# Optimization experiments

Measured on AMD Instinct MI355X. Metric: run time of the kernel, lower is better.

## Reference

```python
import jax, jax.numpy as jnp
import numpy as np

EMBD = 256
HEAD = 4
HD = EMBD // HEAD  # 64
EPS = 1e-5


def setup_inputs() -> dict:
    key = jax.random.key(0)
    ks = jax.random.split(key, 12)
    s = lambda fan_in: 1.0 / np.sqrt(fan_in)
    return {
        "x": jax.random.normal(ks[0], (16, 1024, EMBD), dtype=jnp.float32),
        # attention params (stored as [in, out])
        "qkv_w": jax.random.uniform(ks[1], (EMBD, 3 * EMBD), jnp.float32, -s(EMBD), s(EMBD)),
        "qkv_b": jax.random.uniform(ks[2], (3 * EMBD,), jnp.float32, -s(EMBD), s(EMBD)),
        "out_w": jax.random.uniform(ks[3], (EMBD, EMBD), jnp.float32, -s(EMBD), s(EMBD)),
        "out_b": jax.random.uniform(ks[4], (EMBD,), jnp.float32, -s(EMBD), s(EMBD)),
        # MLP params
        "fc_w": jax.random.uniform(ks[5], (EMBD, 4 * EMBD), jnp.float32, -s(EMBD), s(EMBD)),
        "fc_b": jax.random.uniform(ks[6], (4 * EMBD,), jnp.float32, -s(EMBD), s(EMBD)),
        "proj_w": jax.random.uniform(ks[7], (4 * EMBD, EMBD), jnp.float32, -s(4 * EMBD), s(4 * EMBD)),
        "proj_b": jax.random.uniform(ks[8], (EMBD,), jnp.float32, -s(4 * EMBD), s(4 * EMBD)),
        # LayerNorm params
        "ln1_g": jnp.ones((EMBD,), jnp.float32),
        "ln1_b": jnp.zeros((EMBD,), jnp.float32),
        "ln2_g": jnp.ones((EMBD,), jnp.float32),
        "ln2_b": jnp.zeros((EMBD,), jnp.float32),
    }


def layer_norm(x, g, b):
    mu = jnp.mean(x, axis=-1, keepdims=True)
    var = jnp.mean(jnp.square(x - mu), axis=-1, keepdims=True)
    return (x - mu) * jax.lax.rsqrt(var + EPS) * g + b


def block_forward(x, qkv_w, qkv_b, out_w, out_b, fc_w, fc_b, proj_w, proj_b,
                  ln1_g, ln1_b, ln2_g, ln2_b):
    B, S, E = x.shape
    # --- attention branch ---
    h = layer_norm(x, ln1_g, ln1_b)
    qkv = h @ qkv_w + qkv_b                       # [B,S,3E]
    q, k, v = jnp.split(qkv, 3, axis=-1)
    q = q.reshape(B, S, HEAD, HD).transpose(0, 2, 1, 3)  # [B,H,S,D]
    k = k.reshape(B, S, HEAD, HD).transpose(0, 2, 1, 3)
    v = v.reshape(B, S, HEAD, HD).transpose(0, 2, 1, 3)
    att = jnp.einsum('bhqd,bhkd->bhqk', q, k) / jnp.sqrt(jnp.float32(HD))
    causal = jnp.tril(jnp.ones((S, S), dtype=bool))
    att = jnp.where(causal, att, -jnp.inf)
    att = jax.nn.softmax(att, axis=-1)
    o = jnp.einsum('bhqk,bhkd->bhqd', att, v)     # [B,H,S,D]
    o = o.transpose(0, 2, 1, 3).reshape(B, S, E)
    x = x + o @ out_w + out_b
    # --- MLP branch (dropout inactive at eval) ---
    h = layer_norm(x, ln2_g, ln2_b)
    h = jax.nn.relu(h @ fc_w + fc_b)
    x = x + h @ proj_w + proj_b
    return x


def reference(x, qkv_w, qkv_b, out_w, out_b, fc_w, fc_b, proj_w, proj_b,
              ln1_g, ln1_b, ln2_g, ln2_b):
    return block_forward(x, qkv_w, qkv_b, out_w, out_b, fc_w, fc_b,
                         proj_w, proj_b, ln1_g, ln1_b, ln2_g, ln2_b)
```

## Files before the change

### kernel.cpp

```cpp
#include <hip/hip_runtime.h>
#include <cstdint>


using f32x4 = __attribute__((ext_vector_type(4))) float;
using s16x8 = __attribute__((ext_vector_type(8))) short;
using s16x4 = __attribute__((ext_vector_type(4))) short;

__device__ inline short f2bf(float f) {
    union { float f; unsigned u; } v{f};
    unsigned r = (v.u + 0x7FFFu + ((v.u >> 16) & 1u)) >> 16;
    return (short)r;
}

__device__ inline int cvt_pk_bf16(float lo, float hi) {
    int d;
    asm("v_cvt_pk_bf16_f32 %0, %1, %2" : "=v"(d) : "v"(lo), "v"(hi));
    return d;
}
__device__ inline void swap32(int& a, int& b) {
    asm("v_permlane32_swap_b32 %0, %1" : "+v"(a), "+v"(b));
}
__device__ inline void swap16(int& a, int& b) {
    asm("v_permlane16_swap_b32 %0, %1" : "+v"(a), "+v"(b));
}

__device__ inline void gload16(const void* g, void* l) {
    __builtin_amdgcn_global_load_lds(
        (const __attribute__((address_space(1))) void*)g,
        (__attribute__((address_space(3))) void*)l, 16, 0, 0);
}

__global__ __launch_bounds__(256) void wconv_all_kernel(
    const float* __restrict__ qkv_w, const float* __restrict__ out_w,
    const float* __restrict__ fc_w,  const float* __restrict__ proj_w,
    short* __restrict__ wt_qkv, short* __restrict__ wt_out,
    short* __restrict__ wt_fc,  short* __restrict__ wt_proj)
{
    __shared__ short T[64][65];
    int id = blockIdx.x;
    const float* W; short* Wt; int K, N, nt, kt;
    if (id < 48)       { W = qkv_w;  Wt = wt_qkv;  K = 256;  N = 768;  nt = id % 12;        kt = id / 12; }
    else if (id < 64)  { W = out_w;  Wt = wt_out;  K = 256;  N = 256;  nt = (id - 48) & 3;  kt = (id - 48) >> 2; }
    else if (id < 128) { W = fc_w;   Wt = wt_fc;   K = 256;  N = 1024; nt = (id - 64) & 15; kt = (id - 64) >> 4; }
    else               { W = proj_w; Wt = wt_proj; K = 1024; N = 256;  nt = (id - 128) & 3; kt = (id - 128) >> 2; }
    int n0 = nt * 64, k0 = kt * 64;

    int tid = threadIdx.x;
    int r  = tid >> 2;
    int c  = (tid & 3) << 4;

    const float* src = W + (size_t)(k0 + r) * N + n0 + c;
#pragma unroll
    for (int u = 0; u < 4; ++u) {
        float4 v = *reinterpret_cast<const float4*>(src + u * 4);
        T[r][c + u * 4 + 0] = f2bf(v.x);
        T[r][c + u * 4 + 1] = f2bf(v.y);
        T[r][c + u * 4 + 2] = f2bf(v.z);
        T[r][c + u * 4 + 3] = f2bf(v.w);
    }
    __syncthreads();
    s16x8 o0, o1;
#pragma unroll
    for (int j = 0; j < 8; ++j) { o0[j] = T[c + j][r]; o1[j] = T[c + 8 + j][r]; }
    short* dst = Wt + (size_t)(n0 + r) * K + k0 + c;
    *reinterpret_cast<s16x8*>(dst)     = o0;
    *reinterpret_cast<s16x8*>(dst + 8) = o1;
}

__global__ __launch_bounds__(256) void ln_kernel(const float* __restrict__ x,
                                                 const float* __restrict__ gamma,
                                                 const float* __restrict__ beta,
                                                 short* __restrict__ out)
{
    int tid  = threadIdx.x;
    int lane = tid & 63;
    int row  = blockIdx.x * 4 + (tid >> 6);
    const float* xr = x + (size_t)row * 256;
    float4 v = *reinterpret_cast<const float4*>(xr + lane * 4);

    float s = v.x + v.y + v.z + v.w;
#pragma unroll
    for (int o = 32; o >= 1; o >>= 1) s += __shfl_xor(s, o);
    float mu = s * (1.0f / 256.0f);

    float dx = v.x - mu, dy = v.y - mu, dz = v.z - mu, dw = v.w - mu;
    float q = dx * dx + dy * dy + dz * dz + dw * dw;
#pragma unroll
    for (int o = 32; o >= 1; o >>= 1) q += __shfl_xor(q, o);
    float rstd = rsqrtf(q * (1.0f / 256.0f) + 1e-5f);

    float4 gv = *reinterpret_cast<const float4*>(gamma + lane * 4);
    float4 bv = *reinterpret_cast<const float4*>(beta + lane * 4);
    s16x4 ov;
    ov[0] = f2bf(dx * rstd * gv.x + bv.x);
    ov[1] = f2bf(dy * rstd * gv.y + bv.y);
    ov[2] = f2bf(dz * rstd * gv.z + bv.z);
    ov[3] = f2bf(dw * rstd * gv.w + bv.w);
    *reinterpret_cast<s16x4*>(out + (size_t)row * 256 + lane * 4) = ov;
}

template <int RELU, int RES, int OBF16, int BM, int QKV>
__global__ __launch_bounds__(256) void mgemm_kernel(const short* __restrict__ A,
                                                    const short* __restrict__ Bt,
                                                    const float* __restrict__ bias,
                                                    const float* __restrict__ R,
                                                    void* __restrict__ Cv,
                                                    short* __restrict__ vt,
                                                    int N, int K)
{
    constexpr int MI  = BM / 32;
    constexpr int ASZ = BM * 64;
    constexpr int BSZ = 128 * 64;
    __shared__ short As[2 * ASZ];
    __shared__ short Bs[2 * BSZ];

    int tid = threadIdx.x;
    int l   = tid & 63;
    int w   = tid >> 6;
    int lr  = l & 15;
    int lk8 = (l >> 4) << 3;
    int r4  = (l >> 4) << 2;
    int wr  = w >> 1, wc = w & 1;
    int bn  = blockIdx.x * 128, bm = blockIdx.y * BM;

    int scolS = ((l & 7) << 3) ^ ((l >> 3) << 3);
    int srowA = w * (BM / 4) + (l >> 3);
    int srowB = (w << 5) + (l >> 3);
    const short* pa = A  + (size_t)(bm + srowA) * K + scolS;
    const short* pb = Bt + (size_t)(bn + srowB) * K + scolS;
    short* dstA = As + w * (BM / 4) * 64;
    short* dstB = Bs + (w << 11);

    f32x4 acc[MI][4];
#pragma unroll
    for (int mi = 0; mi < MI; ++mi)
#pragma unroll
        for (int ni = 0; ni < 4; ++ni) acc[mi][ni] = (f32x4){0.f, 0.f, 0.f, 0.f};

    int swz = (lr & 7) << 3;

#pragma unroll
    for (int i = 0; i < BM / 32; ++i)
        gload16(pa + (size_t)(i * 8) * K, dstA + (i << 9));
#pragma unroll
    for (int i = 0; i < 4; ++i)
        gload16(pb + (size_t)(i * 8) * K, dstB + (i << 9));
    __syncthreads();

    int cur = 0;
    for (int k0 = 0; k0 < K; k0 += 64) {
        if (k0 + 64 < K) {
            int nxt = cur ^ 1;
#pragma unroll
            for (int i = 0; i < BM / 32; ++i)
                gload16(pa + (size_t)(i * 8) * K + k0 + 64, dstA + nxt * ASZ + (i << 9));
#pragma unroll
            for (int i = 0; i < 4; ++i)
                gload16(pb + (size_t)(i * 8) * K + k0 + 64, dstB + nxt * BSZ + (i << 9));
        }
        const short* curA = As + cur * ASZ;
        const short* curB = Bs + cur * BSZ;
#pragma unroll
        for (int ks = 0; ks < 2; ++ks) {
            s16x8 af[MI], bf[4];
#pragma unroll
            for (int mi = 0; mi < MI; ++mi) {
                int row = wr * (BM / 2) + (mi << 4) + lr;
                af[mi] = *reinterpret_cast<const s16x8*>(
                    &curA[(row << 6) + (((ks << 5) + lk8) ^ swz)]);
            }
#pragma unroll
            for (int ni = 0; ni < 4; ++ni) {
                int row = (wc << 6) + (ni << 4) + lr;
                bf[ni] = *reinterpret_cast<const s16x8*>(
                    &curB[(row << 6) + (((ks << 5) + lk8) ^ swz)]);
            }
            __builtin_amdgcn_s_setprio(1);
#pragma unroll
            for (int mi = 0; mi < MI; ++mi)
#pragma unroll
                for (int ni = 0; ni < 4; ++ni)
                    acc[mi][ni] = __builtin_amdgcn_mfma_f32_16x16x32_bf16(
                        af[mi], bf[ni], acc[mi][ni], 0, 0, 0);
            __builtin_amdgcn_s_setprio(0);
        }
        __syncthreads();
        cur ^= 1;
    }

    float bv[4];
#pragma unroll
    for (int ni = 0; ni < 4; ++ni)
        bv[ni] = bias[bn + (wc << 6) + (ni << 4) + lr];

#pragma unroll
    for (int mi = 0; mi < MI; ++mi) {
#pragma unroll
        for (int ni = 0; ni < 4; ++ni) {
            int n = bn + (wc << 6) + (ni << 4) + lr;
#pragma unroll
            for (int r = 0; r < 4; ++r) {
                int m = bm + wr * (BM / 2) + (mi << 4) + r4 + r;
                float v = acc[mi][ni][r] + bv[ni];
                if (RELU) v = fmaxf(v, 0.0f);
                if (RES)  v += R[(size_t)m * N + n];
                if (QKV) {
                    if (bn < 512) {
                        ((short*)Cv)[(size_t)m * 512 + n] = f2bf(v);
                    } else {
                        int hh = (n - 512) >> 6, dd = (n - 512) & 63;
                        int bb = m >> 10, ss = m & 1023;
                        vt[(size_t)((((bb << 2) | hh) << 6) | dd) * 1024 + ss] = f2bf(v);
                    }
                } else if (OBF16) {
                    ((short*)Cv)[(size_t)m * N + n] = f2bf(v);
                } else {
                    ((float*)Cv)[(size_t)m * N + n] = v;
                }
            }
        }
    }
}

__global__ __launch_bounds__(256) void oproj_ln_kernel(const short* __restrict__ A,
                                                       const short* __restrict__ Bt,
                                                       const float* __restrict__ bias,
                                                       const float* __restrict__ R,
                                                       float* __restrict__ x1,
                                                       short* __restrict__ h2,
                                                       const float* __restrict__ g,
                                                       const float* __restrict__ bb)
{
    constexpr int ASZ = 64 * 64;
    constexpr int BSZ = 256 * 64;
    __shared__ short As[2 * ASZ];
    __shared__ short Bs[2 * BSZ];

    int tid = threadIdx.x;
    int l   = tid & 63;
    int w   = tid >> 6;
    int lr  = l & 15;
    int lk8 = (l >> 4) << 3;
    int r4  = (l >> 4) << 2;
    int bm  = blockIdx.x * 64;

    int scolS = ((l & 7) << 3) ^ ((l >> 3) << 3);
    const short* pa = A  + (size_t)(bm + (w << 4) + (l >> 3)) * 256 + scolS;
    const short* pb = Bt + (size_t)((w << 6) + (l >> 3)) * 256 + scolS;
    short* dstA = As + (w << 10);
    short* dstB = Bs + (w << 12);

    f32x4 acc[16];
#pragma unroll
    for (int ni = 0; ni < 16; ++ni) acc[ni] = (f32x4){0.f, 0.f, 0.f, 0.f};

    int swz = (lr & 7) << 3;

#pragma unroll
    for (int i = 0; i < 2; ++i)
        gload16(pa + (size_t)(i * 8) * 256, dstA + (i << 9));
#pragma unroll
    for (int i = 0; i < 8; ++i)
        gload16(pb + (size_t)(i * 8) * 256, dstB + (i << 9));
    __syncthreads();

    int cur = 0;
    for (int k0 = 0; k0 < 256; k0 += 64) {
        if (k0 + 64 < 256) {
            int nxt = cur ^ 1;
#pragma unroll
            for (int i = 0; i < 2; ++i)
                gload16(pa + (size_t)(i * 8) * 256 + k0 + 64, dstA + nxt * ASZ + (i << 9));
#pragma unroll
            for (int i = 0; i < 8; ++i)
                gload16(pb + (size_t)(i * 8) * 256 + k0 + 64, dstB + nxt * BSZ + (i << 9));
        }
        const short* curA = As + cur * ASZ;
        const short* curB = Bs + cur * BSZ;
#pragma unroll
        for (int ks = 0; ks < 2; ++ks) {
            int arow = (w << 4) + lr;
            s16x8 af = *reinterpret_cast<const s16x8*>(
                &curA[(arow << 6) + (((ks << 5) + lk8) ^ swz)]);
            __builtin_amdgcn_s_setprio(1);
#pragma unroll
            for (int ni = 0; ni < 16; ++ni) {
                int row = (ni << 4) + lr;
                s16x8 bf = *reinterpret_cast<const s16x8*>(
                    &curB[(row << 6) + (((ks << 5) + lk8) ^ swz)]);
                acc[ni] = __builtin_amdgcn_mfma_f32_16x16x32_bf16(af, bf, acc[ni], 0, 0, 0);
            }
            __builtin_amdgcn_s_setprio(0);
        }
        __syncthreads();
        cur ^= 1;
    }

#pragma unroll
    for (int ni = 0; ni < 16; ++ni) {
        int n = (ni << 4) + lr;
        float bvx = bias[n];
#pragma unroll
        for (int r = 0; r < 4; ++r) {
            int m = bm + (w << 4) + r4 + r;
            acc[ni][r] += bvx + R[(size_t)m * 256 + n];
        }
    }
#pragma unroll
    for (int r = 0; r < 4; ++r) {
        float s = 0.0f;
#pragma unroll
        for (int ni = 0; ni < 16; ++ni) s += acc[ni][r];
        s += __shfl_xor(s, 1); s += __shfl_xor(s, 2);
        s += __shfl_xor(s, 4); s += __shfl_xor(s, 8);
        float mu = s * (1.0f / 256.0f);
        float q = 0.0f;
#pragma unroll
        for (int ni = 0; ni < 16; ++ni) {
            float d = acc[ni][r] - mu;
            q += d * d;
        }
        q += __shfl_xor(q, 1); q += __shfl_xor(q, 2);
        q += __shfl_xor(q, 4); q += __shfl_xor(q, 8);
        float rstd = rsqrtf(q * (1.0f / 256.0f) + 1e-5f);

        int m = bm + (w << 4) + r4 + r;
#pragma unroll
        for (int ni = 0; ni < 16; ++ni) {
            int n = (ni << 4) + lr;
            float v = acc[ni][r];
            x1[(size_t)m * 256 + n] = v;
            h2[(size_t)m * 256 + n] = f2bf((v - mu) * rstd * g[n] + bb[n]);
        }
    }
}

__global__ __launch_bounds__(256, 4) void attn_kernel(const short* __restrict__ qk,
                                                      const short* __restrict__ vt,
                                                      short* __restrict__ o)
{
    __shared__ short Ks[2][64 * 64];
    __shared__ short Vs[2][64 * 64];

    int bid  = blockIdx.x;
    int xcd  = bid & 7;
    int rest = bid >> 3;
    int tq   = rest & 15;
    int flip = (rest >> 5) & 1;
    int qt   = flip ? 15 - tq : tq;
    int bhg  = rest >> 4;
    int bh   = (bhg << 3) | xcd;
    int b = bh >> 2, h = bh & 3;

    int tid = threadIdx.x;
    int l   = tid & 63;
    int w   = tid >> 6;
    int lr  = l & 15;
    int g   = l >> 4;
    int lk8 = g << 3;
    int w16 = w << 4;

    int srow = (w << 3) + (l >> 3);
    int scol = ((l & 7) << 3) ^ (((l >> 3) & 7) << 3);
    const short* kgp = qk + (size_t)(b * 1024 + srow) * 512 + 256 + h * 64 + scol;
    const short* vgp = vt + (size_t)((bh << 6) + srow) * 1024 + scol;
    short* dstK = &Ks[0][(w << 3) * 64];
    short* dstV = &Vs[0][(w << 3) * 64];
    const int BUFS = 64 * 64;

    const float SC = 0.125f * 1.44269504088896f;
    int rsw = (lr & 7) << 3;

    const short* qrow = qk + (size_t)(b * 1024 + qt * 64 + w16 + lr) * 512 + h * 64;
    s16x8 qf[2];
    qf[0] = *reinterpret_cast<const s16x8*>(qrow + lk8);
    qf[1] = *reinterpret_cast<const s16x8*>(qrow + 32 + lk8);

#pragma unroll
    for (int i = 0; i < 2; ++i) {
        gload16(kgp + (size_t)(i * 32) * 512, dstK + (i << 11));
        gload16(vgp + (size_t)(i * 32) * 1024, dstV + (i << 11));
    }
    __syncthreads();

    float m = -1e30f, lsum = 0.0f;
    f32x4 oacc[4];
#pragma unroll
    for (int dt = 0; dt < 4; ++dt) oacc[dt] = (f32x4){0.f, 0.f, 0.f, 0.f};
    int qglob = qt * 64 + w16 + lr;
    int cur = 0;

    for (int kt = 0; kt <= qt; ++kt) {
        if (kt < qt) {
            int nxt = cur ^ 1;
#pragma unroll
            for (int i = 0; i < 2; ++i) {
                gload16(kgp + (size_t)((kt + 1) * 64 + i * 32) * 512,
                        dstK + nxt * BUFS + (i << 11));
                gload16(vgp + (size_t)(i * 32) * 1024 + (kt + 1) * 64,
                        dstV + nxt * BUFS + (i << 11));
            }
        }

        f32x4 s[4];
#pragma unroll
        for (int jt = 0; jt < 4; ++jt) s[jt] = (f32x4){0.f, 0.f, 0.f, 0.f};
        __builtin_amdgcn_s_setprio(1);
#pragma unroll
        for (int ks = 0; ks < 2; ++ks) {
#pragma unroll
            for (int jt = 0; jt < 4; ++jt) {
                int row = jt * 16 + lr;
                s16x8 kf = *reinterpret_cast<const s16x8*>(
                    &Ks[cur][(row << 6) + ((32 * ks + lk8) ^ rsw)]);
                s[jt] = __builtin_amdgcn_mfma_f32_16x16x32_bf16(kf, qf[ks], s[jt], 0, 0, 0);
            }
        }
        __builtin_amdgcn_s_setprio(0);
#pragma unroll
        for (int jt = 0; jt < 4; ++jt)
#pragma unroll
            for (int r = 0; r < 4; ++r) s[jt][r] *= SC;

        if (kt == qt) {
#pragma unroll
            for (int jt = 0; jt < 4; ++jt) {
                int kb = kt * 64 + jt * 16 + (g << 2);
#pragma unroll
                for (int r = 0; r < 4; ++r)
                    if (kb + r > qglob) s[jt][r] = -1e30f;
            }
        }

        float rm = fmaxf(fmaxf(s[0][0], s[0][1]), fmaxf(s[0][2], s[0][3]));
#pragma unroll
        for (int jt = 1; jt < 4; ++jt)
            rm = fmaxf(rm, fmaxf(fmaxf(s[jt][0], s[jt][1]), fmaxf(s[jt][2], s[jt][3])));
        rm = fmaxf(rm, __shfl_xor(rm, 16));
        rm = fmaxf(rm, __shfl_xor(rm, 32));
        bool big = __any(rm > m + 8.0f);
        float fct = 1.0f;
        if (big) {
            float mn = fmaxf(m, rm);
            fct = exp2f(m - mn);
            m = mn;
        }
        float ps = 0.0f;
#pragma unroll
        for (int jt = 0; jt < 4; ++jt)
#pragma unroll
            for (int r = 0; r < 4; ++r) {
                float p = exp2f(s[jt][r] - m);
                s[jt][r] = p;
                ps += p;
            }
        ps += __shfl_xor(ps, 16);
        ps += __shfl_xor(ps, 32);
        lsum = lsum * fct + ps;

        int cpk[4][2];
#pragma unroll
        for (int jt = 0; jt < 4; ++jt) {
            cpk[jt][0] = cvt_pk_bf16(s[jt][0], s[jt][1]);
            cpk[jt][1] = cvt_pk_bf16(s[jt][2], s[jt][3]);
        }

        if (big) {
#pragma unroll
            for (int r = 0; r < 4; ++r) {
                float f4 = __shfl(fct, 4 * g + r);
#pragma unroll
                for (int dt = 0; dt < 4; ++dt) oacc[dt][r] *= f4;
            }
        }

#pragma unroll
        for (int ks = 0; ks < 2; ++ks) {
            int a0 = cpk[2 * ks][0],     a1 = cpk[2 * ks][1];
            int b0 = cpk[2 * ks + 1][0], b1 = cpk[2 * ks + 1][1];
            swap32(a0, b0); swap32(a1, b1);
            swap16(a0, b0); swap16(a1, b1);
            union { int i[4]; s16x8 v; } fr;
            fr.i[0] = a0; fr.i[1] = a1; fr.i[2] = b0; fr.i[3] = b1;
            __builtin_amdgcn_s_setprio(1);
#pragma unroll
            for (int dt = 0; dt < 4; ++dt) {
                int row = dt * 16 + lr;
                s16x8 vf = *reinterpret_cast<const s16x8*>(
                    &Vs[cur][(row << 6) + ((32 * ks + lk8) ^ rsw)]);
                oacc[dt] = __builtin_amdgcn_mfma_f32_16x16x32_bf16(fr.v, vf, oacc[dt], 0, 0, 0);
            }
            __builtin_amdgcn_s_setprio(0);
        }

        if (kt < qt) {
            __syncthreads();
            cur ^= 1;
        }
    }

#pragma unroll
    for (int r = 0; r < 4; ++r) {
        float lv  = __shfl(lsum, 4 * g + r);
        float inv = 1.0f / lv;
        short* orow = o + (size_t)(b * 1024 + qt * 64 + w16 + 4 * g + r) * 256 + h * 64;
#pragma unroll
        for (int dt = 0; dt < 4; ++dt)
            orow[dt * 16 + lr] = f2bf(oacc[dt][r] * inv);
    }
}

extern "C" void kernel_launch(void* const* d_in, const int* in_sizes, int n_in,
                              void* d_out, int out_size, void* d_ws, size_t ws_size,
                              hipStream_t stream)
{
    const float* x      = (const float*)d_in[0];
    const float* qkv_w  = (const float*)d_in[1];
    const float* qkv_b  = (const float*)d_in[2];
    const float* out_w  = (const float*)d_in[3];
    const float* out_b  = (const float*)d_in[4];
    const float* fc_w   = (const float*)d_in[5];
    const float* fc_b   = (const float*)d_in[6];
    const float* proj_w = (const float*)d_in[7];
    const float* proj_b = (const float*)d_in[8];
    const float* ln1_g  = (const float*)d_in[9];
    const float* ln1_b  = (const float*)d_in[10];
    const float* ln2_g  = (const float*)d_in[11];
    const float* ln2_b  = (const float*)d_in[12];
    float* out = (float*)d_out;

    short* ws = (short*)d_ws;
    short* wt_qkv  = ws;
    short* wt_out  = ws + 196608;
    short* wt_fc   = ws + 262144;
    short* wt_proj = ws + 524288;
    short* bufA    = ws + 786432;
    short* qk_buf  = ws + 4980736;
    short* vt_buf  = ws + 13369344;
    short* h3_buf  = ws + 4980736;

    dim3 blk(256);

    wconv_all_kernel<<<dim3(192), blk, 0, stream>>>(
        qkv_w, out_w, fc_w, proj_w, wt_qkv, wt_out, wt_fc, wt_proj);
    ln_kernel<<<dim3(4096), blk, 0, stream>>>(x, ln1_g, ln1_b, bufA);
    mgemm_kernel<0, 0, 1, 128, 1><<<dim3(6, 128), blk, 0, stream>>>(
        bufA, wt_qkv, qkv_b, nullptr, qk_buf, vt_buf, 768, 256);
    attn_kernel<<<dim3(1024), blk, 0, stream>>>(qk_buf, vt_buf, bufA);
    oproj_ln_kernel<<<dim3(256), blk, 0, stream>>>(
        bufA, wt_out, out_b, x, out, bufA, ln2_g, ln2_b);
    mgemm_kernel<1, 0, 1, 128, 0><<<dim3(8, 128), blk, 0, stream>>>(
        bufA, wt_fc, fc_b, nullptr, h3_buf, nullptr, 1024, 256);
    mgemm_kernel<0, 1, 0, 64, 0><<<dim3(2, 256), blk, 0, stream>>>(
        h3_buf, wt_proj, proj_b, out, out, nullptr, 256, 1024);
}
```

Baseline: 132.3 us.

## Merge weight prep with LN1, single-buffer K=256 GEMMs, retile attention with 32x32 MFMA

The weight-transpose and first LayerNorm kernels are merged into one launch, removing a kernel launch. The GEMM gains a DBUF template flag: the K=256 GEMMs now use a single LDS buffer to lower LDS use and raise occupancy, while the proj GEMM keeps double buffering. Attention is retiled to 128-query by 128-key blocks using 32x32x16 MFMAs, halving the grid and improving K/V reuse. The cost is lower attention occupancy (launch bounds 2), coarser causal load balance, and exposed load latency in the single-buffered GEMMs.

```diff
diff --git a/kernel.cpp b/kernel.cpp
--- a/kernel.cpp
+++ b/kernel.cpp
@@ -2,9 +2,10 @@
 #include <cstdint>
 
 
-using f32x4 = __attribute__((ext_vector_type(4))) float;
-using s16x8 = __attribute__((ext_vector_type(8))) short;
-using s16x4 = __attribute__((ext_vector_type(4))) short;
+using f32x4  = __attribute__((ext_vector_type(4))) float;
+using f32x16 = __attribute__((ext_vector_type(16))) float;
+using s16x8  = __attribute__((ext_vector_type(8))) short;
+using s16x4  = __attribute__((ext_vector_type(4))) short;
 
 __device__ inline short f2bf(float f) {
     union { float f; unsigned u; } v{f};
@@ -20,9 +21,6 @@
 __device__ inline void swap32(int& a, int& b) {
     asm("v_permlane32_swap_b32 %0, %1" : "+v"(a), "+v"(b));
 }
-__device__ inline void swap16(int& a, int& b) {
-    asm("v_permlane16_swap_b32 %0, %1" : "+v"(a), "+v"(b));
-}
 
 __device__ inline void gload16(const void* g, void* l) {
     __builtin_amdgcn_global_load_lds(
@@ -30,76 +28,68 @@
         (__attribute__((address_space(3))) void*)l, 16, 0, 0);
 }
 
-__global__ __launch_bounds__(256) void wconv_all_kernel(
+__global__ __launch_bounds__(256) void prep_kernel(
     const float* __restrict__ qkv_w, const float* __restrict__ out_w,
     const float* __restrict__ fc_w,  const float* __restrict__ proj_w,
     short* __restrict__ wt_qkv, short* __restrict__ wt_out,
-    short* __restrict__ wt_fc,  short* __restrict__ wt_proj)
+    short* __restrict__ wt_fc,  short* __restrict__ wt_proj,
+    const float* __restrict__ x, const float* __restrict__ ln1_g,
+    const float* __restrict__ ln1_b, short* __restrict__ hout)
 {
     __shared__ short T[64][65];
-    int id = blockIdx.x;
-    const float* W; short* Wt; int K, N, nt, kt;
-    if (id < 48)       { W = qkv_w;  Wt = wt_qkv;  K = 256;  N = 768;  nt = id % 12;        kt = id / 12; }
-    else if (id < 64)  { W = out_w;  Wt = wt_out;  K = 256;  N = 256;  nt = (id - 48) & 3;  kt = (id - 48) >> 2; }
-    else if (id < 128) { W = fc_w;   Wt = wt_fc;   K = 256;  N = 1024; nt = (id - 64) & 15; kt = (id - 64) >> 4; }
-    else               { W = proj_w; Wt = wt_proj; K = 1024; N = 256;  nt = (id - 128) & 3; kt = (id - 128) >> 2; }
-    int n0 = nt * 64, k0 = kt * 64;
-
+    int id  = blockIdx.x;
     int tid = threadIdx.x;
-    int r  = tid >> 2;
-    int c  = (tid & 3) << 4;
-
-    const float* src = W + (size_t)(k0 + r) * N + n0 + c;
-#pragma unroll
-    for (int u = 0; u < 4; ++u) {
-        float4 v = *reinterpret_cast<const float4*>(src + u * 4);
-        T[r][c + u * 4 + 0] = f2bf(v.x);
-        T[r][c + u * 4 + 1] = f2bf(v.y);
-        T[r][c + u * 4 + 2] = f2bf(v.z);
-        T[r][c + u * 4 + 3] = f2bf(v.w);
-    }
-    __syncthreads();
-    s16x8 o0, o1;
-#pragma unroll
-    for (int j = 0; j < 8; ++j) { o0[j] = T[c + j][r]; o1[j] = T[c + 8 + j][r]; }
-    short* dst = Wt + (size_t)(n0 + r) * K + k0 + c;
-    *reinterpret_cast<s16x8*>(dst)     = o0;
-    *reinterpret_cast<s16x8*>(dst + 8) = o1;
-}
-
-__global__ __launch_bounds__(256) void ln_kernel(const float* __restrict__ x,
-                                                 const float* __restrict__ gamma,
-                                                 const float* __restrict__ beta,
-                                                 short* __restrict__ out)
-{
-    int tid  = threadIdx.x;
-    int lane = tid & 63;
-    int row  = blockIdx.x * 4 + (tid >> 6);
-    const float* xr = x + (size_t)row * 256;
-    float4 v = *reinterpret_cast<const float4*>(xr + lane * 4);
-
-    float s = v.x + v.y + v.z + v.w;
-#pragma unroll
-    for (int o = 32; o >= 1; o >>= 1) s += __shfl_xor(s, o);
-    float mu = s * (1.0f / 256.0f);
-
-    float dx = v.x - mu, dy = v.y - mu, dz = v.z - mu, dw = v.w - mu;
-    float q = dx * dx + dy * dy + dz * dz + dw * dw;
-#pragma unroll
-    for (int o = 32; o >= 1; o >>= 1) q += __shfl_xor(q, o);
-    float rstd = rsqrtf(q * (1.0f / 256.0f) + 1e-5f);
-
-    float4 gv = *reinterpret_cast<const float4*>(gamma + lane * 4);
-    float4 bv = *reinterpret_cast<const float4*>(beta + lane * 4);
-    s16x4 ov;
-    ov[0] = f2bf(dx * rstd * gv.x + bv.x);
-    ov[1] = f2bf(dy * rstd * gv.y + bv.y);
-    ov[2] = f2bf(dz * rstd * gv.z + bv.z);
-    ov[3] = f2bf(dw * rstd * gv.w + bv.w);
-    *reinterpret_cast<s16x4*>(out + (size_t)row * 256 + lane * 4) = ov;
-}
-
-template <int RELU, int RES, int OBF16, int BM, int QKV>
+
+    if (id < 192) {
+        const float* W; short* Wt; int K, N, nt, kt;
+        if (id < 48)       { W = qkv_w;  Wt = wt_qkv;  K = 256;  N = 768;  nt = id % 12;        kt = id / 12; }
+        else if (id < 64)  { W = out_w;  Wt = wt_out;  K = 256;  N = 256;  nt = (id - 48) & 3;  kt = (id - 48) >> 2; }
+        else if (id < 128) { W = fc_w;   Wt = wt_fc;   K = 256;  N = 1024; nt = (id - 64) & 15; kt = (id - 64) >> 4; }
+        else               { W = proj_w; Wt = wt_proj; K = 1024; N = 256;  nt = (id - 128) & 3; kt = (id - 128) >> 2; }
+        int n0 = nt * 64, k0 = kt * 64;
+        int r = tid >> 2, c = (tid & 3) << 4;
+        const float* src = W + (size_t)(k0 + r) * N + n0 + c;
+#pragma unroll
+        for (int u = 0; u < 4; ++u) {
+            float4 v = *reinterpret_cast<const float4*>(src + u * 4);
+            T[r][c + u * 4 + 0] = f2bf(v.x);
+            T[r][c + u * 4 + 1] = f2bf(v.y);
+            T[r][c + u * 4 + 2] = f2bf(v.z);
+            T[r][c + u * 4 + 3] = f2bf(v.w);
+        }
+        __syncthreads();
+        s16x8 o0, o1;
+#pragma unroll
+        for (int jj = 0; jj < 8; ++jj) { o0[jj] = T[c + jj][r]; o1[jj] = T[c + 8 + jj][r]; }
+        short* dst = Wt + (size_t)(n0 + r) * K + k0 + c;
+        *reinterpret_cast<s16x8*>(dst)     = o0;
+        *reinterpret_cast<s16x8*>(dst + 8) = o1;
+    } else {
+        int lane = tid & 63;
+        int row  = (id - 192) * 4 + (tid >> 6);
+        const float* xr = x + (size_t)row * 256;
+        float4 v = *reinterpret_cast<const float4*>(xr + lane * 4);
+        float s = v.x + v.y + v.z + v.w;
+#pragma unroll
+        for (int o2 = 32; o2 >= 1; o2 >>= 1) s += __shfl_xor(s, o2);
+        float mu = s * (1.0f / 256.0f);
+        float dx = v.x - mu, dy = v.y - mu, dz = v.z - mu, dw = v.w - mu;
+        float q = dx * dx + dy * dy + dz * dz + dw * dw;
+#pragma unroll
+        for (int o2 = 32; o2 >= 1; o2 >>= 1) q += __shfl_xor(q, o2);
+        float rstd = rsqrtf(q * (1.0f / 256.0f) + 1e-5f);
+        float4 gv = *reinterpret_cast<const float4*>(ln1_g + lane * 4);
+        float4 bv = *reinterpret_cast<const float4*>(ln1_b + lane * 4);
+        s16x4 ov;
+        ov[0] = f2bf(dx * rstd * gv.x + bv.x);
+        ov[1] = f2bf(dy * rstd * gv.y + bv.y);
+        ov[2] = f2bf(dz * rstd * gv.z + bv.z);
+        ov[3] = f2bf(dw * rstd * gv.w + bv.w);
+        *reinterpret_cast<s16x4*>(hout + (size_t)row * 256 + lane * 4) = ov;
+    }
+}
+
+template <int RELU, int RES, int OBF16, int BM, int QKV, int DBUF>
 __global__ __launch_bounds__(256) void mgemm_kernel(const short* __restrict__ A,
                                                     const short* __restrict__ Bt,
                                                     const float* __restrict__ bias,
@@ -111,8 +101,8 @@
     constexpr int MI  = BM / 32;
     constexpr int ASZ = BM * 64;
     constexpr int BSZ = 128 * 64;
-    __shared__ short As[2 * ASZ];
-    __shared__ short Bs[2 * BSZ];
+    __shared__ short As[(1 + DBUF) * ASZ];
+    __shared__ short Bs[(1 + DBUF) * BSZ];
 
     int tid = threadIdx.x;
     int l   = tid & 63;
@@ -138,25 +128,38 @@
         for (int ni = 0; ni < 4; ++ni) acc[mi][ni] = (f32x4){0.f, 0.f, 0.f, 0.f};
 
     int swz = (lr & 7) << 3;
-
-#pragma unroll
-    for (int i = 0; i < BM / 32; ++i)
-        gload16(pa + (size_t)(i * 8) * K, dstA + (i << 9));
-#pragma unroll
-    for (int i = 0; i < 4; ++i)
-        gload16(pb + (size_t)(i * 8) * K, dstB + (i << 9));
-    __syncthreads();
-
     int cur = 0;
+
+    if (DBUF) {
+#pragma unroll
+        for (int i = 0; i < BM / 32; ++i)
+            gload16(pa + (size_t)(i * 8) * K, dstA + (i << 9));
+#pragma unroll
+        for (int i = 0; i < 4; ++i)
+            gload16(pb + (size_t)(i * 8) * K, dstB + (i << 9));
+        __syncthreads();
+    }
+
     for (int k0 = 0; k0 < K; k0 += 64) {
-        if (k0 + 64 < K) {
-            int nxt = cur ^ 1;
+        if (DBUF) {
+            if (k0 + 64 < K) {
+                int nxt = cur ^ 1;
+#pragma unroll
+                for (int i = 0; i < BM / 32; ++i)
+                    gload16(pa + (size_t)(i * 8) * K + k0 + 64, dstA + nxt * ASZ + (i << 9));
+#pragma unroll
+                for (int i = 0; i < 4; ++i)
+                    gload16(pb + (size_t)(i * 8) * K + k0 + 64, dstB + nxt * BSZ + (i << 9));
+            }
+        } else {
+            __syncthreads();
 #pragma unroll
             for (int i = 0; i < BM / 32; ++i)
-                gload16(pa + (size_t)(i * 8) * K + k0 + 64, dstA + nxt * ASZ + (i << 9));
+                gload16(pa + (size_t)(i * 8) * K + k0, dstA + (i << 9));
 #pragma unroll
             for (int i = 0; i < 4; ++i)
-                gload16(pb + (size_t)(i * 8) * K + k0 + 64, dstB + nxt * BSZ + (i << 9));
+                gload16(pb + (size_t)(i * 8) * K + k0, dstB + (i << 9));
+            __syncthreads();
         }
         const short* curA = As + cur * ASZ;
         const short* curB = Bs + cur * BSZ;
@@ -184,8 +187,10 @@
                         af[mi], bf[ni], acc[mi][ni], 0, 0, 0);
             __builtin_amdgcn_s_setprio(0);
         }
-        __syncthreads();
-        cur ^= 1;
+        if (DBUF) {
+            __syncthreads();
+            cur ^= 1;
+        }
     }
 
     float bv[4];
@@ -335,108 +340,114 @@
     }
 }
 
-__global__ __launch_bounds__(256, 4) void attn_kernel(const short* __restrict__ qk,
+__global__ __launch_bounds__(256, 2) void attn_kernel(const short* __restrict__ qk,
                                                       const short* __restrict__ vt,
                                                       short* __restrict__ o)
 {
-    __shared__ short Ks[2][64 * 64];
-    __shared__ short Vs[2][64 * 64];
+    constexpr int KSZ = 128 * 64;
+    constexpr int VSZ = 64 * 128;
+    __shared__ short Ks[2 * KSZ];
+    __shared__ short Vs[2 * VSZ];
 
     int bid  = blockIdx.x;
     int xcd  = bid & 7;
-    int rest = bid >> 3;
-    int tq   = rest & 15;
-    int flip = (rest >> 5) & 1;
-    int qt   = flip ? 15 - tq : tq;
-    int bhg  = rest >> 4;
+    int j    = bid >> 3;
+    int bhg  = j & 7;
+    int qidx = j >> 3;
+    int qt   = qidx < 4 ? qidx : 11 - qidx;
     int bh   = (bhg << 3) | xcd;
     int b = bh >> 2, h = bh & 3;
 
     int tid = threadIdx.x;
     int l   = tid & 63;
     int w   = tid >> 6;
-    int lr  = l & 15;
-    int g   = l >> 4;
-    int lk8 = g << 3;
-    int w16 = w << 4;
-
-    int srow = (w << 3) + (l >> 3);
-    int scol = ((l & 7) << 3) ^ (((l >> 3) & 7) << 3);
-    const short* kgp = qk + (size_t)(b * 1024 + srow) * 512 + 256 + h * 64 + scol;
-    const short* vgp = vt + (size_t)((bh << 6) + srow) * 1024 + scol;
-    short* dstK = &Ks[0][(w << 3) * 64];
-    short* dstV = &Vs[0][(w << 3) * 64];
-    const int BUFS = 64 * 64;
+    int lq  = l & 31;
+    int hg  = l >> 5;
+
+    int krow0 = (w << 3) + (l >> 3);
+    int kscol = ((l & 7) << 3) ^ (((l >> 3) & 7) << 3);
+    const short* kgp = qk + (size_t)(b * 1024 + krow0) * 512 + 256 + h * 64 + kscol;
+    short* dstK = Ks + (w << 3) * 64;
+    int vrow0 = (w << 2) + (l >> 4);
+    int vscol = ((l & 15) << 3) ^ ((vrow0 & 7) << 3);
+    const short* vgp = vt + (size_t)((bh << 6) + vrow0) * 1024 + vscol;
+    short* dstV = Vs + (w << 2) * 128;
 
     const float SC = 0.125f * 1.44269504088896f;
-    int rsw = (lr & 7) << 3;
-
-    const short* qrow = qk + (size_t)(b * 1024 + qt * 64 + w16 + lr) * 512 + h * 64;
-    s16x8 qf[2];
-    qf[0] = *reinterpret_cast<const s16x8*>(qrow + lk8);
-    qf[1] = *reinterpret_cast<const s16x8*>(qrow + 32 + lk8);
-
-#pragma unroll
-    for (int i = 0; i < 2; ++i) {
-        gload16(kgp + (size_t)(i * 32) * 512, dstK + (i << 11));
-        gload16(vgp + (size_t)(i * 32) * 1024, dstV + (i << 11));
+
+    const short* qrow = qk + (size_t)(b * 1024 + qt * 128 + (w << 5) + lq) * 512
+                        + h * 64 + (hg << 3);
+    s16x8 qf[4];
+#pragma unroll
+    for (int ds = 0; ds < 4; ++ds)
+        qf[ds] = *reinterpret_cast<const s16x8*>(qrow + 16 * ds);
+
+#pragma unroll
+    for (int i = 0; i < 4; ++i) {
+        gload16(kgp + (size_t)(i * 32) * 512, dstK + i * 32 * 64);
+        gload16(vgp + (size_t)(i * 16) * 1024, dstV + i * 16 * 128);
     }
     __syncthreads();
 
     float m = -1e30f, lsum = 0.0f;
-    f32x4 oacc[4];
-#pragma unroll
-    for (int dt = 0; dt < 4; ++dt) oacc[dt] = (f32x4){0.f, 0.f, 0.f, 0.f};
-    int qglob = qt * 64 + w16 + lr;
+    f32x16 oacc[2];
+#pragma unroll
+    for (int dt = 0; dt < 2; ++dt)
+#pragma unroll
+        for (int r = 0; r < 16; ++r) oacc[dt][r] = 0.0f;
+    int qglob = qt * 128 + (w << 5) + lq;
     int cur = 0;
-
-    for (int kt = 0; kt <= qt; ++kt) {
-        if (kt < qt) {
+    int niter = qt + 1;
+
+    for (int kt = 0; kt < niter; ++kt) {
+        if (kt + 1 < niter) {
             int nxt = cur ^ 1;
 #pragma unroll
-            for (int i = 0; i < 2; ++i) {
-                gload16(kgp + (size_t)((kt + 1) * 64 + i * 32) * 512,
-                        dstK + nxt * BUFS + (i << 11));
-                gload16(vgp + (size_t)(i * 32) * 1024 + (kt + 1) * 64,
-                        dstV + nxt * BUFS + (i << 11));
-            }
-        }
-
-        f32x4 s[4];
-#pragma unroll
-        for (int jt = 0; jt < 4; ++jt) s[jt] = (f32x4){0.f, 0.f, 0.f, 0.f};
+            for (int i = 0; i < 4; ++i) {
+                gload16(kgp + (size_t)((kt + 1) * 128 + i * 32) * 512,
+                        dstK + nxt * KSZ + i * 32 * 64);
+                gload16(vgp + (size_t)(i * 16) * 1024 + (kt + 1) * 128,
+                        dstV + nxt * VSZ + i * 16 * 128);
+            }
+        }
+
+        f32x16 sv[4];
+#pragma unroll
+        for (int jt = 0; jt < 4; ++jt)
+#pragma unroll
+            for (int r = 0; r < 16; ++r) sv[jt][r] = 0.0f;
         __builtin_amdgcn_s_setprio(1);
 #pragma unroll
-        for (int ks = 0; ks < 2; ++ks) {
+        for (int ds = 0; ds < 4; ++ds) {
 #pragma unroll
             for (int jt = 0; jt < 4; ++jt) {
-                int row = jt * 16 + lr;
+                int row = jt * 32 + lq;
                 s16x8 kf = *reinterpret_cast<const s16x8*>(
-                    &Ks[cur][(row << 6) + ((32 * ks + lk8) ^ rsw)]);
-                s[jt] = __builtin_amdgcn_mfma_f32_16x16x32_bf16(kf, qf[ks], s[jt], 0, 0, 0);
+                    &Ks[cur * KSZ + (row << 6) + ((16 * ds + (hg << 3)) ^ ((row & 7) << 3))]);
+                sv[jt] = __builtin_amdgcn_mfma_f32_32x32x16_bf16(kf, qf[ds], sv[jt], 0, 0, 0);
             }
         }
         __builtin_amdgcn_s_setprio(0);
 #pragma unroll
         for (int jt = 0; jt < 4; ++jt)
 #pragma unroll
-            for (int r = 0; r < 4; ++r) s[jt][r] *= SC;
-
-        if (kt == qt) {
-#pragma unroll
-            for (int jt = 0; jt < 4; ++jt) {
-                int kb = kt * 64 + jt * 16 + (g << 2);
-#pragma unroll
-                for (int r = 0; r < 4; ++r)
-                    if (kb + r > qglob) s[jt][r] = -1e30f;
-            }
-        }
-
-        float rm = fmaxf(fmaxf(s[0][0], s[0][1]), fmaxf(s[0][2], s[0][3]));
-#pragma unroll
-        for (int jt = 1; jt < 4; ++jt)
-            rm = fmaxf(rm, fmaxf(fmaxf(s[jt][0], s[jt][1]), fmaxf(s[jt][2], s[jt][3])));
-        rm = fmaxf(rm, __shfl_xor(rm, 16));
+            for (int r = 0; r < 16; ++r) sv[jt][r] *= SC;
+
+        if (kt == niter - 1) {
+#pragma unroll
+            for (int jt = 0; jt < 4; ++jt)
+#pragma unroll
+                for (int r = 0; r < 16; ++r) {
+                    int kg = kt * 128 + jt * 32 + (r & 3) + ((r >> 2) << 3) + (hg << 2);
+                    if (kg > qglob) sv[jt][r] = -1e30f;
+                }
+        }
+
+        float rm = -1e30f;
+#pragma unroll
+        for (int jt = 0; jt < 4; ++jt)
+#pragma unroll
+            for (int r = 0; r < 16; ++r) rm = fmaxf(rm, sv[jt][r]);
         rm = fmaxf(rm, __shfl_xor(rm, 32));
         bool big = __any(rm > m + 8.0f);
         float fct = 1.0f;
@@ -449,64 +460,68 @@
 #pragma unroll
         for (int jt = 0; jt < 4; ++jt)
 #pragma unroll
-            for (int r = 0; r < 4; ++r) {
-                float p = exp2f(s[jt][r] - m);
-                s[jt][r] = p;
+            for (int r = 0; r < 16; ++r) {
+                float p = exp2f(sv[jt][r] - m);
+                sv[jt][r] = p;
                 ps += p;
             }
-        ps += __shfl_xor(ps, 16);
         ps += __shfl_xor(ps, 32);
         lsum = lsum * fct + ps;
 
-        int cpk[4][2];
+        if (big) {
+#pragma unroll
+            for (int r = 0; r < 16; ++r) {
+                float f = __shfl(fct, (r & 3) + ((r >> 2) << 3) + (hg << 2));
+                oacc[0][r] *= f;
+                oacc[1][r] *= f;
+            }
+        }
+
 #pragma unroll
         for (int jt = 0; jt < 4; ++jt) {
-            cpk[jt][0] = cvt_pk_bf16(s[jt][0], s[jt][1]);
-            cpk[jt][1] = cvt_pk_bf16(s[jt][2], s[jt][3]);
-        }
-
-        if (big) {
-#pragma unroll
-            for (int r = 0; r < 4; ++r) {
-                float f4 = __shfl(fct, 4 * g + r);
-#pragma unroll
-                for (int dt = 0; dt < 4; ++dt) oacc[dt][r] *= f4;
-            }
-        }
-
-#pragma unroll
-        for (int ks = 0; ks < 2; ++ks) {
-            int a0 = cpk[2 * ks][0],     a1 = cpk[2 * ks][1];
-            int b0 = cpk[2 * ks + 1][0], b1 = cpk[2 * ks + 1][1];
-            swap32(a0, b0); swap32(a1, b1);
-            swap16(a0, b0); swap16(a1, b1);
-            union { int i[4]; s16x8 v; } fr;
-            fr.i[0] = a0; fr.i[1] = a1; fr.i[2] = b0; fr.i[3] = b1;
+            int x0 = cvt_pk_bf16(sv[jt][0],  sv[jt][1]);
+            int x1 = cvt_pk_bf16(sv[jt][2],  sv[jt][3]);
+            int y0 = cvt_pk_bf16(sv[jt][4],  sv[jt][5]);
+            int y1 = cvt_pk_bf16(sv[jt][6],  sv[jt][7]);
+            int z0 = cvt_pk_bf16(sv[jt][8],  sv[jt][9]);
+            int z1 = cvt_pk_bf16(sv[jt][10], sv[jt][11]);
+            int w0 = cvt_pk_bf16(sv[jt][12], sv[jt][13]);
+            int w1 = cvt_pk_bf16(sv[jt][14], sv[jt][15]);
+            swap32(x0, y0); swap32(x1, y1);
+            swap32(z0, w0); swap32(z1, w1);
+            union { int i[4]; s16x8 v; } fA, fB;
+            fA.i[0] = x0; fA.i[1] = x1; fA.i[2] = y0; fA.i[3] = y1;
+            fB.i[0] = z0; fB.i[1] = z1; fB.i[2] = w0; fB.i[3] = w1;
             __builtin_amdgcn_s_setprio(1);
 #pragma unroll
-            for (int dt = 0; dt < 4; ++dt) {
-                int row = dt * 16 + lr;
-                s16x8 vf = *reinterpret_cast<const s16x8*>(
-                    &Vs[cur][(row << 6) + ((32 * ks + lk8) ^ rsw)]);
-                oacc[dt] = __builtin_amdgcn_mfma_f32_16x16x32_bf16(fr.v, vf, oacc[dt], 0, 0, 0);
+            for (int dt = 0; dt < 2; ++dt) {
+                int row = dt * 32 + lq;
+                int rs  = (row & 7) << 3;
+                s16x8 vfA = *reinterpret_cast<const s16x8*>(
+                    &Vs[cur * VSZ + (row << 7) + ((16 * (2 * jt)     + (hg << 3)) ^ rs)]);
+                oacc[dt] = __builtin_amdgcn_mfma_f32_32x32x16_bf16(fA.v, vfA, oacc[dt], 0, 0, 0);
+                s16x8 vfB = *reinterpret_cast<const s16x8*>(
+                    &Vs[cur * VSZ + (row << 7) + ((16 * (2 * jt + 1) + (hg << 3)) ^ rs)]);
+                oacc[dt] = __builtin_amdgcn_mfma_f32_32x32x16_bf16(fB.v, vfB, oacc[dt], 0, 0, 0);
             }
             __builtin_amdgcn_s_setprio(0);
         }
 
-        if (kt < qt) {
+        if (kt + 1 < niter) {
             __syncthreads();
             cur ^= 1;
         }
     }
 
 #pragma unroll
-    for (int r = 0; r < 4; ++r) {
-        float lv  = __shfl(lsum, 4 * g + r);
+    for (int r = 0; r < 16; ++r) {
+        int qr  = (r & 3) + ((r >> 2) << 3) + (hg << 2);
+        float lv  = __shfl(lsum, qr);
         float inv = 1.0f / lv;
-        short* orow = o + (size_t)(b * 1024 + qt * 64 + w16 + 4 * g + r) * 256 + h * 64;
-#pragma unroll
-        for (int dt = 0; dt < 4; ++dt)
-            orow[dt * 16 + lr] = f2bf(oacc[dt][r] * inv);
+        int q = qt * 128 + (w << 5) + qr;
+        short* orow = o + (size_t)(b * 1024 + q) * 256 + h * 64;
+        orow[lq]      = f2bf(oacc[0][r] * inv);
+        orow[32 + lq] = f2bf(oacc[1][r] * inv);
     }
 }
 
@@ -541,16 +556,16 @@
 
     dim3 blk(256);
 
-    wconv_all_kernel<<<dim3(192), blk, 0, stream>>>(
-        qkv_w, out_w, fc_w, proj_w, wt_qkv, wt_out, wt_fc, wt_proj);
-    ln_kernel<<<dim3(4096), blk, 0, stream>>>(x, ln1_g, ln1_b, bufA);
-    mgemm_kernel<0, 0, 1, 128, 1><<<dim3(6, 128), blk, 0, stream>>>(
+    prep_kernel<<<dim3(4288), blk, 0, stream>>>(
+        qkv_w, out_w, fc_w, proj_w, wt_qkv, wt_out, wt_fc, wt_proj,
+        x, ln1_g, ln1_b, bufA);
+    mgemm_kernel<0, 0, 1, 128, 1, 0><<<dim3(6, 128), blk, 0, stream>>>(
         bufA, wt_qkv, qkv_b, nullptr, qk_buf, vt_buf, 768, 256);
-    attn_kernel<<<dim3(1024), blk, 0, stream>>>(qk_buf, vt_buf, bufA);
+    attn_kernel<<<dim3(512), blk, 0, stream>>>(qk_buf, vt_buf, bufA);
     oproj_ln_kernel<<<dim3(256), blk, 0, stream>>>(
         bufA, wt_out, out_b, x, out, bufA, ln2_g, ln2_b);
-    mgemm_kernel<1, 0, 1, 128, 0><<<dim3(8, 128), blk, 0, stream>>>(
+    mgemm_kernel<1, 0, 1, 128, 0, 0><<<dim3(8, 128), blk, 0, stream>>>(
         bufA, wt_fc, fc_b, nullptr, h3_buf, nullptr, 1024, 256);
-    mgemm_kernel<0, 1, 0, 64, 0><<<dim3(2, 256), blk, 0, stream>>>(
+    mgemm_kernel<0, 1, 0, 64, 0, 1><<<dim3(2, 256), blk, 0, stream>>>(
         h3_buf, wt_proj, proj_b, out, out, nullptr, 256, 1024);
 }
```

Measured after the change: 119.3 us. 1.11x faster.
